# Kernel tuning notes

Measured on AMD Instinct MI355X. Metric: run time of the kernel, lower is better.

## Reference

```python
import jax, jax.numpy as jnp
import numpy as np
import math

N_H = 16

def _rope(x):
    # x: [b, h, n, d_k]; standard RoPE with half-split rotation
    n, d_k = x.shape[2], x.shape[3]
    inv_freq = 1.0 / (10000.0 ** (jnp.arange(0, d_k, 2, dtype=jnp.float32) / d_k))  # [d_k/2]
    freqs = jnp.arange(n, dtype=jnp.float32)[:, None] * inv_freq[None, :]            # [n, d_k/2]
    cos = jnp.concatenate([jnp.cos(freqs), jnp.cos(freqs)], axis=-1)[None, None]     # [1,1,n,d_k]
    sin = jnp.concatenate([jnp.sin(freqs), jnp.sin(freqs)], axis=-1)[None, None]
    x1, x2 = jnp.split(x, 2, axis=-1)
    rot = jnp.concatenate([-x2, x1], axis=-1)
    return x * cos + rot * sin


def setup_inputs() -> dict:
    key = jax.random.key(0)
    k1, k2, k3, k4 = jax.random.split(key, 4)
    b, n, d_m = 2, 1024, 2048
    x = jax.random.normal(k1, (b, n, d_m), dtype=jnp.float32)
    # causal mask (1 = keep, 0 = masked)
    m = jnp.tril(jnp.ones((n, n), dtype=jnp.int32))[None, None]  # [1,1,n,n]
    s = 1.0 / math.sqrt(d_m)
    Wqkv = jax.random.normal(k2, (d_m, 3 * d_m), dtype=jnp.float32) * s
    Wout = jax.random.normal(k3, (d_m, d_m), dtype=jnp.float32) * s
    bout = jax.random.normal(k4, (d_m,), dtype=jnp.float32) * 0.01
    return {"x": x, "m": m, "Wqkv": Wqkv, "Wout": Wout, "bout": bout}


def reference(x, m, Wqkv, Wout, bout):
    b, n, d = x.shape
    d_k = d // N_H
    qkv = (x @ Wqkv).reshape(b, n, 3, N_H, d_k)
    qkv = jnp.transpose(qkv, (2, 0, 3, 1, 4))  # [3, b, h, n, d_k]
    q, k, v = qkv[0], qkv[1], qkv[2]
    q, k = _rope(q), _rope(k)
    s = jnp.einsum('bhqd,bhkd->bhqk', q, k) / math.sqrt(d_k)
    s = jnp.where(m == 0, -jnp.inf, s)
    a = jax.nn.softmax(s, axis=-1)  # dropout is identity in eval / drop=0
    r = jnp.einsum('bhqk,bhkd->bhqd', a, v)
    r = jnp.transpose(r, (0, 2, 1, 3)).reshape(b, n, d)
    return r @ Wout + bout
```

## Files before the change

### kernel.cpp

```cpp
#include <hip/hip_runtime.h>
#include <math.h>

typedef unsigned short u16;
typedef unsigned int u32;
typedef __attribute__((ext_vector_type(8))) short short8;
typedef __attribute__((ext_vector_type(4))) float f32x4;

#define DEVI __device__ __forceinline__

DEVI u16 f2bf(float x) {
    union { float f; u32 u; } un; un.f = x;
    u32 u = un.u;
    return (u16)((u + 0x7fffu + ((u >> 16) & 1u)) >> 16);
}
DEVI u32 cvtpk(float lo, float hi) {
    u32 r;
    asm("v_cvt_pk_bf16_f32 %0, %1, %2" : "=v"(r) : "v"(lo), "v"(hi));
    return r;
}
DEVI float bf2f(u16 v) {
    union { u32 u; float f; } un; un.u = ((u32)v) << 16;
    return un.f;
}
DEVI f32x4 mfma_bf16(short8 a, short8 b, f32x4 c) {
    return __builtin_amdgcn_mfma_f32_16x16x32_bf16(a, b, c, 0, 0, 0);
}
DEVI void gload_lds16(const void* g, void* l) {
    __builtin_amdgcn_global_load_lds((const __attribute__((address_space(1))) u32*)g,
                                     (__attribute__((address_space(3))) u32*)l,
                                     16, 0, 0);
}

__global__ void k_prep(const float* __restrict__ x, const float* __restrict__ Wqkv,
                       const float* __restrict__ Wout, u16* __restrict__ x_bf,
                       u16* __restrict__ WqkvT, u16* __restrict__ WoutT) {
    __shared__ u16 tile[64][68];
    const int bid = blockIdx.x;
    if (bid < 4096) {
        long idx = ((long)bid * 256 + threadIdx.x) * 4;
        float4 v = *(const float4*)(x + idx);
        uint2 o;
        o.x = cvtpk(v.x, v.y);
        o.y = cvtpk(v.z, v.w);
        *(uint2*)(x_bf + idx) = o;
        return;
    }
    const float* in;
    u16* out;
    int R, C, bx, by;
    if (bid < 7168) {
        int lb = bid - 4096;
        in = Wqkv; out = WqkvT; R = 2048; C = 6144;
        bx = lb % 96; by = lb / 96;
    } else {
        int lb = bid - 7168;
        in = Wout; out = WoutT; R = 2048; C = 2048;
        bx = lb & 31; by = lb >> 5;
    }
    const int tx = threadIdx.x & 15, ty = threadIdx.x >> 4;
    const long r0 = (long)by * 64, c0 = (long)bx * 64;
#pragma unroll
    for (int p = 0; p < 4; ++p) {
        int r = ty + p * 16;
        float4 v = *(const float4*)(in + (r0 + r) * C + c0 + tx * 4);
        uint2 o;
        o.x = cvtpk(v.x, v.y);
        o.y = cvtpk(v.z, v.w);
        *(uint2*)&tile[r][tx * 4] = o;
    }
    __syncthreads();
#pragma unroll
    for (int p = 0; p < 4; ++p) {
        int rr = ty + p * 16;
        ushort4 o;
        o.x = tile[tx * 4 + 0][rr];
        o.y = tile[tx * 4 + 1][rr];
        o.z = tile[tx * 4 + 2][rr];
        o.w = tile[tx * 4 + 3][rr];
        *(ushort4*)(out + (c0 + rr) * R + r0 + tx * 4) = o;
    }
}

template <int EPI, int TM>
__global__ __launch_bounds__(256, 3) void k_gemm(const u16* __restrict__ A,
                                                 const u16* __restrict__ BT, int K,
                                                 u16* __restrict__ qb, u16* __restrict__ kb,
                                                 u16* __restrict__ vtb, float* __restrict__ out,
                                                 const float* __restrict__ bias) {
    constexpr int MI = TM / 32;
    constexpr int CA = TM / 32;
    __shared__ __align__(16) union SM {
        struct { u16 As[TM * 64]; u16 Bs[128 * 64]; } s;
        u16 T[EPI == 0 ? 128 * 132 : 8];
    } sm;
    const int tid = threadIdx.x;
    const int lane = tid & 63, wave = tid >> 6;
    const int lm = lane & 15, quad = lane >> 4;
    const int wm = wave >> 1, wn = wave & 1;
    const int nwg = gridDim.x * gridDim.y;
    const int lin = blockIdx.y * gridDim.x + blockIdx.x;
    const int work = (lin & 7) * (nwg >> 3) + (lin >> 3);
    const int bm = work % gridDim.x, bn = work / gridDim.x;

    f32x4 acc[MI][4] = {};

    const int srow = lane >> 3;
    const int scb = (lane & 7) ^ srow;
    const long arow0 = (long)bm * TM;
    const long brow0 = (long)bn * 128;

    for (int k0 = 0; k0 < K; k0 += 64) {
        __syncthreads();
#pragma unroll
        for (int it = 0; it < CA; ++it) {
            int ch = wave * CA + it;
            long r = ch * 8 + srow;
            gload_lds16(A + (arow0 + r) * K + k0 + scb * 8, (char*)sm.s.As + ch * 1024);
        }
#pragma unroll
        for (int it = 0; it < 4; ++it) {
            int ch = wave * 4 + it;
            long r = ch * 8 + srow;
            gload_lds16(BT + (brow0 + r) * K + k0 + scb * 8, (char*)sm.s.Bs + ch * 1024);
        }
        __syncthreads();
#pragma unroll
        for (int ko = 0; ko < 2; ++ko) {
            short8 af[MI], bf[4];
#pragma unroll
            for (int i = 0; i < MI; ++i) {
                int row = wm * (TM / 2) + i * 16 + lm;
                int pc = (ko * 4 + quad) ^ (lm & 7);
                af[i] = *(const short8*)&sm.s.As[row * 64 + pc * 8];
            }
#pragma unroll
            for (int j = 0; j < 4; ++j) {
                int row = wn * 64 + j * 16 + lm;
                int pc = (ko * 4 + quad) ^ (lm & 7);
                bf[j] = *(const short8*)&sm.s.Bs[row * 64 + pc * 8];
            }
#pragma unroll
            for (int i = 0; i < MI; ++i)
#pragma unroll
                for (int j = 0; j < 4; ++j)
                    acc[i][j] = mfma_bf16(af[i], bf[j], acc[i][j]);
        }
    }

    if constexpr (EPI == 0) {
        __syncthreads();
#pragma unroll
        for (int i = 0; i < MI; ++i)
#pragma unroll
            for (int j = 0; j < 4; ++j) {
                const int col = wn * 64 + j * 16 + lm;
                const int row0 = wm * 64 + i * 16 + quad * 4;
                const u32 p01 = cvtpk(acc[i][j][0], acc[i][j][1]);
                const u32 p23 = cvtpk(acc[i][j][2], acc[i][j][3]);
                sm.T[(row0 + 0) * 132 + col] = (u16)p01;
                sm.T[(row0 + 1) * 132 + col] = (u16)(p01 >> 16);
                sm.T[(row0 + 2) * 132 + col] = (u16)p23;
                sm.T[(row0 + 3) * 132 + col] = (u16)(p23 >> 16);
            }
        __syncthreads();
        const int which = bn >> 4, h = bn & 15, b = bm >> 3;
        const int p0 = (bm & 7) * 128;
        if (which < 2) {
            u16* dst = which ? kb : qb;
            const long hb = ((long)(b * 16 + h)) * 1024;
            const int i0 = (tid * 4) & 63;
            const int pb = tid >> 4;
            float inv[4];
#pragma unroll
            for (int e = 0; e < 4; ++e)
                inv[e] = exp2f(-(float)(i0 + e) * 0.20762050593045952f);
#pragma unroll
            for (int c = 0; c < 8; ++c) {
                const int pos_l = c * 16 + pb;
                ushort4 cur = *(const ushort4*)&sm.T[pos_l * 132 + i0];
                ushort4 par = *(const ushort4*)&sm.T[pos_l * 132 + i0 + 64];
                const float pg = (float)(p0 + pos_l);
                const u16* cp = (const u16*)&cur;
                const u16* pp = (const u16*)&par;
                float f1[4], f2[4];
#pragma unroll
                for (int e = 0; e < 4; ++e) {
                    float th = pg * inv[e];
                    float sv = __sinf(th), cv = __cosf(th);
                    float x1 = bf2f(cp[e]), x2 = bf2f(pp[e]);
                    f1[e] = x1 * cv - x2 * sv;
                    f2[e] = x2 * cv + x1 * sv;
                }
                uint2 o1, o2;
                o1.x = cvtpk(f1[0], f1[1]); o1.y = cvtpk(f1[2], f1[3]);
                o2.x = cvtpk(f2[0], f2[1]); o2.y = cvtpk(f2[2], f2[3]);
                const long rowb = (hb + p0 + pos_l) * 128;
                *(uint2*)(dst + rowb + i0) = o1;
                *(uint2*)(dst + rowb + i0 + 64) = o2;
            }
        } else {
            const long vrow = ((long)(b * 16 + h)) * 128;
#pragma unroll
            for (int c = 0; c < 8; ++c) {
                const int lin2 = c * 2048 + tid * 8;
                const int dk = lin2 >> 7;
                const int ps = lin2 & 127;
                ushort4 o1, o2;
                u16* o1p = (u16*)&o1;
                u16* o2p = (u16*)&o2;
#pragma unroll
                for (int e = 0; e < 4; ++e) {
                    o1p[e] = sm.T[(ps + e) * 132 + dk];
                    o2p[e] = sm.T[(ps + 4 + e) * 132 + dk];
                }
                u16* dst = vtb + (vrow + dk) * 1024 + p0 + ps;
                *(ushort4*)dst = o1;
                *(ushort4*)(dst + 4) = o2;
            }
        }
    } else {
        float bv[4];
#pragma unroll
        for (int j = 0; j < 4; ++j) bv[j] = bias[bn * 128 + wn * 64 + j * 16 + lm];
#pragma unroll
        for (int i = 0; i < MI; ++i) {
#pragma unroll
            for (int r = 0; r < 4; ++r) {
                const int row = bm * TM + wm * (TM / 2) + i * 16 + quad * 4 + r;
#pragma unroll
                for (int j = 0; j < 4; ++j) {
                    const int col = bn * 128 + wn * 64 + j * 16 + lm;
                    out[(long)row * 2048 + col] = acc[i][j][r] + bv[j];
                }
            }
        }
    }
}

__global__ __launch_bounds__(256, 2) void k_flash(const u16* __restrict__ Q,
                                                  const u16* __restrict__ Kb,
                                                  const u16* __restrict__ VT,
                                                  u16* __restrict__ R) {
    __shared__ u16 Ks[2][64 * 128];
    __shared__ u16 Vs[2][128 * 64];
    __shared__ u16 Ps[64 * 72];
    const int tid = threadIdx.x;
    const int lane = tid & 63, wave = tid >> 6;
    const int lm = lane & 15, quad = lane >> 4;
    const int p = blockIdx.x;
    const int half = p >> 8, q8 = p & 255;
    const int xcd = q8 & 7, j8 = q8 >> 3;
    const int bh = xcd * 4 + (j8 >> 3);
    const int s = j8 & 7;
    const int qt = half ? (15 - s) : s;
    const long qkbase = (long)bh * 1024 * 128;
    const long vtbase = (long)bh * 128 * 1024;
    const int q0 = qt * 64;

    short8 qf[4];
    {
        const u16* qrow = Q + qkbase + (long)(q0 + wave * 16 + lm) * 128 + quad * 8;
#pragma unroll
        for (int kc = 0; kc < 4; ++kc) qf[kc] = *(const short8*)(qrow + kc * 32);
    }

    f32x4 o_acc[8] = {};
    float m_i = -INFINITY, l_i = 0.f;
    const float cl2e = 0.08838834764831845f * 1.4426950408889634f;

    const int kr = lane >> 4;
    const int vr = lane >> 3;
    const int vcb = (lane & 7) ^ vr;

    auto stage = [&](int buf, int kt) {
#pragma unroll
        for (int it = 0; it < 4; ++it) {
            int ch = wave * 4 + it;
            int krow = ch * 4 + kr;
            int kchunk = (lane & 15) ^ (krow & 15);
            gload_lds16(Kb + qkbase + (long)(kt * 64 + krow) * 128 + kchunk * 8,
                        (char*)Ks[buf] + ch * 1024);
            int vrow = ch * 8 + vr;
            gload_lds16(VT + vtbase + (long)vrow * 1024 + kt * 64 + vcb * 8,
                        (char*)Vs[buf] + ch * 1024);
        }
    };

    stage(0, 0);
    __syncthreads();
    int cur = 0;

    for (int kt = 0; kt <= qt; ++kt) {
        if (kt < qt) stage(cur ^ 1, kt + 1);
        asm volatile("" ::: "memory");

        f32x4 s_acc[4] = {};
        __builtin_amdgcn_s_setprio(1);
#pragma unroll
        for (int kc = 0; kc < 4; ++kc) {
#pragma unroll
            for (int mi = 0; mi < 4; ++mi) {
                int row = mi * 16 + lm;
                int pc = (kc * 4 + quad) ^ lm;
                short8 ak = *(const short8*)&Ks[cur][row * 128 + pc * 8];
                s_acc[mi] = mfma_bf16(ak, qf[kc], s_acc[mi]);
            }
        }
        __builtin_amdgcn_s_setprio(0);
        float t[4][4];
        float cmax = -INFINITY;
        if (kt < qt) {
#pragma unroll
            for (int mi = 0; mi < 4; ++mi)
#pragma unroll
                for (int r = 0; r < 4; ++r) {
                    float val = s_acc[mi][r] * cl2e;
                    t[mi][r] = val;
                    cmax = fmaxf(cmax, val);
                }
        } else {
            const int qg = q0 + wave * 16 + lm;
#pragma unroll
            for (int mi = 0; mi < 4; ++mi)
#pragma unroll
                for (int r = 0; r < 4; ++r) {
                    int kg = kt * 64 + mi * 16 + quad * 4 + r;
                    float val = (kg <= qg) ? s_acc[mi][r] * cl2e : -INFINITY;
                    t[mi][r] = val;
                    cmax = fmaxf(cmax, val);
                }
        }
        cmax = fmaxf(cmax, __shfl_xor(cmax, 16));
        cmax = fmaxf(cmax, __shfl_xor(cmax, 32));
        float m_new = fmaxf(m_i, cmax);
        const bool defer = __all(cmax - m_i <= 8.f);
        if (defer) m_new = m_i;
        float csum = 0.f;
#pragma unroll
        for (int mi = 0; mi < 4; ++mi)
#pragma unroll
            for (int r = 0; r < 4; ++r) {
                float p2 = exp2f(t[mi][r] - m_new);
                t[mi][r] = p2;
                csum += p2;
            }
        csum += __shfl_xor(csum, 16);
        csum += __shfl_xor(csum, 32);
        if (!defer) {
            float alpha = exp2f(m_i - m_new);
            float aq[4];
#pragma unroll
            for (int r = 0; r < 4; ++r) aq[r] = __shfl(alpha, quad * 4 + r, 64);
#pragma unroll
            for (int nt = 0; nt < 8; ++nt)
#pragma unroll
                for (int r = 0; r < 4; ++r) o_acc[nt][r] *= aq[r];
            l_i = l_i * alpha + csum;
        } else {
            l_i += csum;
        }
        m_i = m_new;
#pragma unroll
        for (int mi = 0; mi < 4; ++mi) {
            uint2 pk2;
            pk2.x = cvtpk(t[mi][0], t[mi][1]);
            pk2.y = cvtpk(t[mi][2], t[mi][3]);
            *(uint2*)&Ps[(wave * 16 + lm) * 72 + mi * 16 + quad * 4] = pk2;
        }
        __builtin_amdgcn_s_setprio(1);
#pragma unroll
        for (int kc = 0; kc < 2; ++kc) {
            short8 ap = *(const short8*)&Ps[(wave * 16 + lm) * 72 + kc * 32 + quad * 8];
#pragma unroll
            for (int nt = 0; nt < 8; ++nt) {
                int row = nt * 16 + lm;
                int pc = (kc * 4 + quad) ^ (lm & 7);
                short8 bv = *(const short8*)&Vs[cur][row * 64 + pc * 8];
                o_acc[nt] = mfma_bf16(ap, bv, o_acc[nt]);
            }
        }
        __builtin_amdgcn_s_setprio(0);
        __syncthreads();
        cur ^= 1;
    }
    float lq[4], il[4];
#pragma unroll
    for (int r = 0; r < 4; ++r) lq[r] = __shfl(l_i, quad * 4 + r, 64);
#pragma unroll
    for (int r = 0; r < 4; ++r) il[r] = 1.0f / lq[r];
    const int b = bh >> 4, h = bh & 15;
    const int pos0 = q0 + wave * 16 + quad * 4;
#pragma unroll
    for (int nt = 0; nt < 8; ++nt) {
        const int col = h * 128 + nt * 16 + lm;
        const u32 p01 = cvtpk(o_acc[nt][0] * il[0], o_acc[nt][1] * il[1]);
        const u32 p23 = cvtpk(o_acc[nt][2] * il[2], o_acc[nt][3] * il[3]);
        R[((long)b * 1024 + pos0 + 0) * 2048 + col] = (u16)p01;
        R[((long)b * 1024 + pos0 + 1) * 2048 + col] = (u16)(p01 >> 16);
        R[((long)b * 1024 + pos0 + 2) * 2048 + col] = (u16)p23;
        R[((long)b * 1024 + pos0 + 3) * 2048 + col] = (u16)(p23 >> 16);
    }
}

extern "C" void kernel_launch(void* const* d_in, const int* in_sizes, int n_in,
                              void* d_out, int out_size, void* d_ws, size_t ws_size,
                              hipStream_t stream) {
    const float* x    = (const float*)d_in[0];
    const float* Wqkv = (const float*)d_in[2];
    const float* Wout = (const float*)d_in[3];
    const float* bout = (const float*)d_in[4];
    float* out = (float*)d_out;

    char* ws = (char*)d_ws;
    u16* x_bf  = (u16*)(ws);
    u16* rbuf  = x_bf;
    u16* WqkvT = (u16*)(ws + (8L << 20));
    u16* WoutT = (u16*)(ws + (32L << 20));
    u16* qbuf  = (u16*)(ws + (40L << 20));
    u16* kbuf  = (u16*)(ws + (48L << 20));
    u16* vtbuf = (u16*)(ws + (56L << 20));

    k_prep<<<8192, 256, 0, stream>>>(x, Wqkv, Wout, x_bf, WqkvT, WoutT);
    k_gemm<0, 128><<<dim3(16, 48), 256, 0, stream>>>(x_bf, WqkvT, 2048, qbuf, kbuf, vtbuf,
                                                     nullptr, nullptr);
    k_flash<<<512, 256, 0, stream>>>(qbuf, kbuf, vtbuf, rbuf);
    k_gemm<1, 64><<<dim3(32, 16), 256, 0, stream>>>(rbuf, WoutT, 2048, nullptr, nullptr,
                                                    nullptr, out, bout);
}
```

Measured before the change: 235.2 us.

## Split-K output projection with atomics and stage flash output through LDS

Replaces the output-projection GEMM (32x16 grid of 64-row tiles) with a split-K kernel using 128x128 tiles. Each block covers half of K and accumulates into a zeroed output with float atomicAdd, giving 512 blocks to fill the CUs. The flash kernel now stages its normalized output tile in shared memory and writes it out with coalesced 16-byte stores instead of scattered 2-byte stores. The cost is an extra memset, atomic traffic on the output, and a summation order that is no longer deterministic.

```diff
diff --git a/kernel.cpp b/kernel.cpp
--- a/kernel.cpp
+++ b/kernel.cpp
@@ -237,6 +237,80 @@
     }
 }
 
+__global__ __launch_bounds__(256, 3) void k_out(const u16* __restrict__ A,
+                                                const u16* __restrict__ BT,
+                                                float* __restrict__ out,
+                                                const float* __restrict__ bias) {
+    __shared__ __align__(16) struct { u16 As[128 * 64]; u16 Bs[128 * 64]; } sm;
+    const int tid = threadIdx.x;
+    const int lane = tid & 63, wave = tid >> 6;
+    const int lm = lane & 15, quad = lane >> 4;
+    const int wm = wave >> 1, wn = wave & 1;
+    const int b = blockIdx.x;
+    const int z = (b >> 3) & 1;
+    const int p = (b >> 4) * 8 + (b & 7);
+    const int bm = p & 15, bn = p >> 4;
+
+    f32x4 acc[4][4] = {};
+    const int srow = lane >> 3;
+    const int scb = (lane & 7) ^ srow;
+    const long arow0 = (long)bm * 128;
+    const long brow0 = (long)bn * 128;
+    const int koff = z * 1024;
+
+    for (int k0 = 0; k0 < 1024; k0 += 64) {
+        __syncthreads();
+#pragma unroll
+        for (int it = 0; it < 4; ++it) {
+            int ch = wave * 4 + it;
+            long r = ch * 8 + srow;
+            gload_lds16(A + (arow0 + r) * 2048 + koff + k0 + scb * 8,
+                        (char*)sm.As + ch * 1024);
+            gload_lds16(BT + (brow0 + r) * 2048 + koff + k0 + scb * 8,
+                        (char*)sm.Bs + ch * 1024);
+        }
+        __syncthreads();
+#pragma unroll
+        for (int ko = 0; ko < 2; ++ko) {
+            short8 af[4], bf[4];
+#pragma unroll
+            for (int i = 0; i < 4; ++i) {
+                int row = wm * 64 + i * 16 + lm;
+                int pc = (ko * 4 + quad) ^ (lm & 7);
+                af[i] = *(const short8*)&sm.As[row * 64 + pc * 8];
+            }
+#pragma unroll
+            for (int j = 0; j < 4; ++j) {
+                int row = wn * 64 + j * 16 + lm;
+                int pc = (ko * 4 + quad) ^ (lm & 7);
+                bf[j] = *(const short8*)&sm.Bs[row * 64 + pc * 8];
+            }
+#pragma unroll
+            for (int i = 0; i < 4; ++i)
+#pragma unroll
+                for (int j = 0; j < 4; ++j)
+                    acc[i][j] = mfma_bf16(af[i], bf[j], acc[i][j]);
+        }
+    }
+
+    float bv[4];
+#pragma unroll
+    for (int j = 0; j < 4; ++j)
+        bv[j] = z ? 0.f : bias[bn * 128 + wn * 64 + j * 16 + lm];
+#pragma unroll
+    for (int i = 0; i < 4; ++i) {
+#pragma unroll
+        for (int r = 0; r < 4; ++r) {
+            const long row = bm * 128 + wm * 64 + i * 16 + quad * 4 + r;
+#pragma unroll
+            for (int j = 0; j < 4; ++j) {
+                const int col = bn * 128 + wn * 64 + j * 16 + lm;
+                atomicAdd(&out[row * 2048 + col], acc[i][j][r] + bv[j]);
+            }
+        }
+    }
+}
+
 __global__ __launch_bounds__(256, 2) void k_flash(const u16* __restrict__ Q,
                                                   const u16* __restrict__ Kb,
                                                   const u16* __restrict__ VT,
@@ -388,17 +462,26 @@
     for (int r = 0; r < 4; ++r) lq[r] = __shfl(l_i, quad * 4 + r, 64);
 #pragma unroll
     for (int r = 0; r < 4; ++r) il[r] = 1.0f / lq[r];
-    const int b = bh >> 4, h = bh & 15;
-    const int pos0 = q0 + wave * 16 + quad * 4;
+    u16* Os = (u16*)Ks;
+    const int row0 = wave * 16 + quad * 4;
 #pragma unroll
     for (int nt = 0; nt < 8; ++nt) {
-        const int col = h * 128 + nt * 16 + lm;
         const u32 p01 = cvtpk(o_acc[nt][0] * il[0], o_acc[nt][1] * il[1]);
         const u32 p23 = cvtpk(o_acc[nt][2] * il[2], o_acc[nt][3] * il[3]);
-        R[((long)b * 1024 + pos0 + 0) * 2048 + col] = (u16)p01;
-        R[((long)b * 1024 + pos0 + 1) * 2048 + col] = (u16)(p01 >> 16);
-        R[((long)b * 1024 + pos0 + 2) * 2048 + col] = (u16)p23;
-        R[((long)b * 1024 + pos0 + 3) * 2048 + col] = (u16)(p23 >> 16);
+        const int col = nt * 16 + lm;
+        Os[(row0 + 0) * 136 + col] = (u16)p01;
+        Os[(row0 + 1) * 136 + col] = (u16)(p01 >> 16);
+        Os[(row0 + 2) * 136 + col] = (u16)p23;
+        Os[(row0 + 3) * 136 + col] = (u16)(p23 >> 16);
+    }
+    __syncthreads();
+    const int b = bh >> 4, h = bh & 15;
+    const long rbase = ((long)b * 1024 + q0) * 2048 + h * 128;
+    const int rr = tid >> 4, c0 = (tid & 15) * 8;
+#pragma unroll
+    for (int pass = 0; pass < 4; ++pass) {
+        const int row = pass * 16 + rr;
+        *(uint4*)(R + rbase + (long)row * 2048 + c0) = *(const uint4*)&Os[row * 136 + c0];
     }
 }
 
@@ -420,10 +503,10 @@
     u16* kbuf  = (u16*)(ws + (48L << 20));
     u16* vtbuf = (u16*)(ws + (56L << 20));
 
+    hipMemsetAsync(out, 0, (size_t)2048 * 2048 * sizeof(float), stream);
     k_prep<<<8192, 256, 0, stream>>>(x, Wqkv, Wout, x_bf, WqkvT, WoutT);
     k_gemm<0, 128><<<dim3(16, 48), 256, 0, stream>>>(x_bf, WqkvT, 2048, qbuf, kbuf, vtbuf,
                                                      nullptr, nullptr);
     k_flash<<<512, 256, 0, stream>>>(qbuf, kbuf, vtbuf, rbuf);
-    k_gemm<1, 64><<<dim3(32, 16), 256, 0, stream>>>(rbuf, WoutT, 2048, nullptr, nullptr,
-                                                    nullptr, out, bout);
-}
+    k_out<<<512, 256, 0, stream>>>(rbuf, WoutT, out, bout);
+}
```

After: 257.2 us. 1.09x slower.
